# Performance work log

Hardware: AMD Instinct MI355X
Metric: run time of the kernel (lower is better)

The kernel has to match this reference:

```python
import jax, jax.numpy as jnp
import numpy as np

N_NODES = 100000


def spmm(edge_src, edge_dst, edge_val, x):
    """z[dst] += val * x[src] over all edges (COO sparse-dense matmul)."""
    gathered = edge_val[:, None] * x[edge_src]  # [E, d]
    return jax.ops.segment_sum(gathered, edge_dst, num_segments=N_NODES)


def setup_inputs() -> dict:
    key = jax.random.key(0)
    k1, k2, k3, k4, k5, k6 = jax.random.split(key, 6)
    N, E, IN, H, C = N_NODES, 1600000, 256, 128, 40
    features = jax.random.normal(k1, (N, IN), dtype=jnp.float32)
    # xavier_uniform-like init
    b1 = float(np.sqrt(6.0 / (IN + H)))
    b2 = float(np.sqrt(6.0 / (H + C)))
    W1 = jax.random.uniform(k2, (IN, H), dtype=jnp.float32, minval=-b1, maxval=b1)
    W2 = jax.random.uniform(k3, (H, C), dtype=jnp.float32, minval=-b2, maxval=b2)
    edge_src = jax.random.randint(k4, (E,), 0, N, dtype=jnp.int32)
    edge_dst = jnp.sort(jax.random.randint(k5, (E,), 0, N, dtype=jnp.int32))
    # normalized-adjacency-like positive edge weights
    edge_val = jax.random.uniform(k6, (E,), dtype=jnp.float32)
    return {"features": features, "W1": W1, "W2": W2,
            "edge_src": edge_src, "edge_dst": edge_dst, "edge_val": edge_val}


def reference(features, W1, W2, edge_src, edge_dst, edge_val):
    # Decoupled GCN: all dense NN layers first (relu between, none after last) ...
    h = jax.nn.relu(features @ W1)
    h = h @ W2  # [N, num_classes]
    # ... then nlayers (=2) rounds of graph propagation (spmm aggregation)
    h = spmm(edge_src, edge_dst, edge_val, h)
    h = spmm(edge_src, edge_dst, edge_val, h)
    return h
```

## Files before the change

kernel.cpp:

```cpp
#include <hip/hip_runtime.h>
#include <cstddef>
#include <cstdint>

#define IN_DIM 256
#define H_DIM  128
#define C_DIM  40
#define BM     128
#define LDQ    68
#define XA_C   32
#define XB_C   8
#define STEP   512

typedef short bf16x8 __attribute__((ext_vector_type(8)));
typedef float f32x16 __attribute__((ext_vector_type(16)));
typedef uint  u32x4  __attribute__((ext_vector_type(4)));

__device__ __forceinline__ ushort f2bf(float f) {
  uint u = __builtin_bit_cast(uint, f);
  u += 0x7fffu + ((u >> 16) & 1u);
  return (ushort)(u >> 16);
}
__device__ __forceinline__ float bf2f(uint s) {
  uint u = s << 16;
  return __builtin_bit_cast(float, u);
}
__device__ __forceinline__ uint pack2bf(float a, float b) {
#if __has_builtin(__builtin_amdgcn_cvt_pk_bf16_f32)
  typedef __bf16 bf16v2 __attribute__((ext_vector_type(2)));
  bf16v2 r = __builtin_amdgcn_cvt_pk_bf16_f32(a, b);
  return __builtin_bit_cast(uint, r);
#else
  return (uint)f2bf(a) | ((uint)f2bf(b) << 16);
#endif
}

__global__ void setup_kernel(const int* __restrict__ dst, int E,
                             int* __restrict__ row_ptr, int N,
                             const float* __restrict__ W1,
                             const float* __restrict__ W2,
                             ushort* __restrict__ b_frag,
                             ushort* __restrict__ w2f) {
  int tid = blockIdx.x * blockDim.x + threadIdx.x;
  if (tid < E) {
    int d1 = dst[tid];
    int d0 = (tid == 0) ? -1 : dst[tid - 1];
    for (int v = d0 + 1; v <= d1; ++v) row_ptr[v] = tid;
    if (tid == E - 1)
      for (int v = d1 + 1; v <= N; ++v) row_ptr[v] = E;
    return;
  }
  int u = tid - E;
  if (u < 4096) {
    int l = u & 63, ks = (u >> 6) & 15, tn = u >> 10;
    int n  = 32 * tn + (l & 31);
    int k0 = ks * 16 + ((l >> 5) << 3);
    ushort r[8];
#pragma unroll
    for (int j = 0; j < 8; ++j) r[j] = f2bf(W1[(k0 + j) * H_DIM + n]);
    *(uint4*)(b_frag + u * 8) = *(uint4*)r;
    return;
  }
  u -= 4096;
  if (u < 1024) {
    int l = u & 63, kt = u >> 6;
    int tn = kt & 1, kb = kt >> 1;
    int n  = 32 * tn + (l & 31);
    int k0 = kb * 16 + ((l >> 5) << 3);
    ushort r[8];
#pragma unroll
    for (int j = 0; j < 8; ++j)
      r[j] = (n < C_DIM) ? f2bf(W2[(k0 + j) * C_DIM + n]) : (ushort)0;
    *(uint4*)(w2f + u * 8) = *(uint4*)r;
  }
}

__global__ __launch_bounds__(256, 4) void fused_dense_kernel(
    const float* __restrict__ feat, const ushort* __restrict__ b_frag,
    const ushort* __restrict__ w2f, ushort* __restrict__ z0a,
    ushort* __restrict__ z0b, int N) {
  __shared__ __align__(16) ushort smem[4 * 32 * LDQ];

  const int t = threadIdx.x;
  const int w = t >> 6, l = t & 63;
  const int nb = blockIdx.x * BM;
  ushort* slab = smem + w * (32 * LDQ);

  const int sr = l >> 4;
  const int sc = l & 15;

  f32x16 acc[4];
#pragma unroll
  for (int tn = 0; tn < 4; ++tn)
#pragma unroll
    for (int r = 0; r < 16; ++r) acc[tn][r] = 0.f;

  const ushort* bp = b_frag + l * 8;
  bf16x8 Bx[2][4];
#pragma unroll
  for (int tn = 0; tn < 4; ++tn)
    Bx[0][tn] = *(const bf16x8*)(bp + tn * (16 * STEP));

  const float* fbase = feat + (size_t)(nb + 32 * w) * IN_DIM + sc * 4;

  float4 pre[8];
#pragma unroll
  for (int c = 0; c < 8; ++c) {
    int grow = nb + 32 * w + 4 * c + sr;
    const float* p = fbase + (size_t)(4 * c + sr) * IN_DIM;
    if (grow >= N) p = feat + (size_t)(N - 1) * IN_DIM + sc * 4;
    pre[c] = *(const float4*)(p);
  }
#pragma unroll
  for (int c = 0; c < 8; ++c) {
    uint2 pk;
    pk.x = pack2bf(pre[c].x, pre[c].y);
    pk.y = pack2bf(pre[c].z, pre[c].w);
    *(uint2*)(slab + (4 * c + sr) * LDQ + sc * 4) = pk;
  }

  const ushort* Abase = slab + (l & 31) * LDQ + ((l >> 5) << 3);

#pragma unroll
  for (int q = 0; q < 4; ++q) {
#pragma unroll
    for (int ks = 0; ks < 4; ++ks) {
      const int gks = 4 * q + ks;
      const int c = gks & 1;
      if (gks < 15) {
#pragma unroll
        for (int tn = 0; tn < 4; ++tn)
          Bx[c ^ 1][tn] = *(const bf16x8*)(bp + tn * (16 * STEP) + (gks + 1) * STEP);
      }
      if (q < 3) {
#pragma unroll
        for (int d = 0; d < 2; ++d) {
          const int cc = 2 * ks + d;
          int grow = nb + 32 * w + 4 * cc + sr;
          const float* p = fbase + (size_t)(4 * cc + sr) * IN_DIM + (q + 1) * 64;
          if (grow >= N) p = feat + (size_t)(N - 1) * IN_DIM + sc * 4 + (q + 1) * 64;
          pre[cc] = *(const float4*)(p);
        }
      }
      bf16x8 af = *(const bf16x8*)(Abase + ks * 16);
#pragma unroll
      for (int tn = 0; tn < 4; ++tn)
        acc[tn] = __builtin_amdgcn_mfma_f32_32x32x16_bf16(af, Bx[c][tn], acc[tn], 0, 0, 0);
    }
    if (q < 3) {
#pragma unroll
      for (int c = 0; c < 8; ++c) {
        uint2 pk;
        pk.x = pack2bf(pre[c].x, pre[c].y);
        pk.y = pack2bf(pre[c].z, pre[c].w);
        *(uint2*)(slab + (4 * c + sr) * LDQ + sc * 4) = pk;
      }
    }
  }

  f32x16 acc2[2];
#pragma unroll
  for (int tn = 0; tn < 2; ++tn)
#pragma unroll
    for (int r = 0; r < 16; ++r) acc2[tn][r] = 0.f;

  const ushort* Hbase = slab + (l & 31) * LDQ + ((l >> 5) << 3);
  const ushort* wp = w2f + l * 8;

#pragma unroll
  for (int hc = 0; hc < 2; ++hc) {
#pragma unroll
    for (int tn = 2 * hc; tn < 2 * hc + 2; ++tn) {
      int col = (tn - 2 * hc) * 32 + (l & 31);
#pragma unroll
      for (int r = 0; r < 16; ++r) {
        int nl = (r & 3) + 8 * (r >> 2) + 4 * (l >> 5);
        float v = acc[tn][r];
        slab[nl * LDQ + col] = f2bf(v > 0.f ? v : 0.f);
      }
    }
#pragma unroll
    for (int kb = 4 * hc; kb < 4 * hc + 4; ++kb) {
      bf16x8 af = *(const bf16x8*)(Hbase + (kb - 4 * hc) * 16);
#pragma unroll
      for (int tn = 0; tn < 2; ++tn) {
        bf16x8 bfr = *(const bf16x8*)(wp + (kb * 2 + tn) * STEP);
        acc2[tn] = __builtin_amdgcn_mfma_f32_32x32x16_bf16(af, bfr, acc2[tn], 0, 0, 0);
      }
    }
  }

#pragma unroll
  for (int r = 0; r < 16; ++r) {
    int node = nb + 32 * w + (r & 3) + 8 * (r >> 2) + 4 * (l >> 5);
    if (node < N) {
      z0a[(size_t)node * XA_C + (l & 31)] = f2bf(acc2[0][r]);
      if ((l & 31) < XB_C)
        z0b[(size_t)node * XB_C + (l & 31)] = f2bf(acc2[1][r]);
    }
  }
}

__global__ __launch_bounds__(256) void spmm_kernel(
    const int* __restrict__ row_ptr, const int* __restrict__ esrc,
    const float* __restrict__ eval, const ushort* __restrict__ xa,
    const ushort* __restrict__ xb, ushort* __restrict__ za,
    ushort* __restrict__ zb8, float* __restrict__ zf, int N, int out_f32) {
  int node = blockIdx.x * 8 + (threadIdx.x >> 5);
  if (node >= N) return;
  const int lh = threadIdx.x & 31;
  const int h = lh >> 2;
  const int j = lh & 3;

  int e   = row_ptr[node];
  int end = row_ptr[node + 1];

  float acc[8], accb[8];
#pragma unroll
  for (int c = 0; c < 8; ++c) { acc[c] = 0.f; accb[c] = 0.f; }

  for (; e + 16 <= end; e += 16) {
    int   s0 = esrc[e + h];
    int   s1 = esrc[e + 8 + h];
    float v0 = eval[e + h];
    float v1 = eval[e + 8 + h];
    u32x4 a = *(const u32x4*)(xa + (size_t)s0 * XA_C + j * 8);
    u32x4 b = *(const u32x4*)(xa + (size_t)s1 * XA_C + j * 8);
    acc[0] = fmaf(v0, bf2f(a.x & 0xffffu), acc[0]);
    acc[1] = fmaf(v0, bf2f(a.x >> 16),     acc[1]);
    acc[2] = fmaf(v0, bf2f(a.y & 0xffffu), acc[2]);
    acc[3] = fmaf(v0, bf2f(a.y >> 16),     acc[3]);
    acc[4] = fmaf(v0, bf2f(a.z & 0xffffu), acc[4]);
    acc[5] = fmaf(v0, bf2f(a.z >> 16),     acc[5]);
    acc[6] = fmaf(v0, bf2f(a.w & 0xffffu), acc[6]);
    acc[7] = fmaf(v0, bf2f(a.w >> 16),     acc[7]);
    acc[0] = fmaf(v1, bf2f(b.x & 0xffffu), acc[0]);
    acc[1] = fmaf(v1, bf2f(b.x >> 16),     acc[1]);
    acc[2] = fmaf(v1, bf2f(b.y & 0xffffu), acc[2]);
    acc[3] = fmaf(v1, bf2f(b.y >> 16),     acc[3]);
    acc[4] = fmaf(v1, bf2f(b.z & 0xffffu), acc[4]);
    acc[5] = fmaf(v1, bf2f(b.z >> 16),     acc[5]);
    acc[6] = fmaf(v1, bf2f(b.w & 0xffffu), acc[6]);
    acc[7] = fmaf(v1, bf2f(b.w >> 16),     acc[7]);
    if (j == 0) {
      u32x4 p = *(const u32x4*)(xb + (size_t)s0 * XB_C);
      u32x4 q = *(const u32x4*)(xb + (size_t)s1 * XB_C);
      accb[0] = fmaf(v0, bf2f(p.x & 0xffffu), accb[0]);
      accb[1] = fmaf(v0, bf2f(p.x >> 16),     accb[1]);
      accb[2] = fmaf(v0, bf2f(p.y & 0xffffu), accb[2]);
      accb[3] = fmaf(v0, bf2f(p.y >> 16),     accb[3]);
      accb[4] = fmaf(v0, bf2f(p.z & 0xffffu), accb[4]);
      accb[5] = fmaf(v0, bf2f(p.z >> 16),     accb[5]);
      accb[6] = fmaf(v0, bf2f(p.w & 0xffffu), accb[6]);
      accb[7] = fmaf(v0, bf2f(p.w >> 16),     accb[7]);
      accb[0] = fmaf(v1, bf2f(q.x & 0xffffu), accb[0]);
      accb[1] = fmaf(v1, bf2f(q.x >> 16),     accb[1]);
      accb[2] = fmaf(v1, bf2f(q.y & 0xffffu), accb[2]);
      accb[3] = fmaf(v1, bf2f(q.y >> 16),     accb[3]);
      accb[4] = fmaf(v1, bf2f(q.z & 0xffffu), accb[4]);
      accb[5] = fmaf(v1, bf2f(q.z >> 16),     accb[5]);
      accb[6] = fmaf(v1, bf2f(q.w & 0xffffu), accb[6]);
      accb[7] = fmaf(v1, bf2f(q.w >> 16),     accb[7]);
    }
  }
  for (; e + 8 <= end; e += 8) {
    int   s = esrc[e + h];
    float v = eval[e + h];
    u32x4 a = *(const u32x4*)(xa + (size_t)s * XA_C + j * 8);
    acc[0] = fmaf(v, bf2f(a.x & 0xffffu), acc[0]);
    acc[1] = fmaf(v, bf2f(a.x >> 16),     acc[1]);
    acc[2] = fmaf(v, bf2f(a.y & 0xffffu), acc[2]);
    acc[3] = fmaf(v, bf2f(a.y >> 16),     acc[3]);
    acc[4] = fmaf(v, bf2f(a.z & 0xffffu), acc[4]);
    acc[5] = fmaf(v, bf2f(a.z >> 16),     acc[5]);
    acc[6] = fmaf(v, bf2f(a.w & 0xffffu), acc[6]);
    acc[7] = fmaf(v, bf2f(a.w >> 16),     acc[7]);
    if (j == 0) {
      u32x4 p = *(const u32x4*)(xb + (size_t)s * XB_C);
      accb[0] = fmaf(v, bf2f(p.x & 0xffffu), accb[0]);
      accb[1] = fmaf(v, bf2f(p.x >> 16),     accb[1]);
      accb[2] = fmaf(v, bf2f(p.y & 0xffffu), accb[2]);
      accb[3] = fmaf(v, bf2f(p.y >> 16),     accb[3]);
      accb[4] = fmaf(v, bf2f(p.z & 0xffffu), accb[4]);
      accb[5] = fmaf(v, bf2f(p.z >> 16),     accb[5]);
      accb[6] = fmaf(v, bf2f(p.w & 0xffffu), accb[6]);
      accb[7] = fmaf(v, bf2f(p.w >> 16),     accb[7]);
    }
  }
  if (e < end) {
    int ei = e + h;
    int ec = ei < end ? ei : end - 1;
    int   s  = esrc[ec];
    float v0 = eval[ec];
    float v  = ei < end ? v0 : 0.f;
    u32x4 a = *(const u32x4*)(xa + (size_t)s * XA_C + j * 8);
    acc[0] = fmaf(v, bf2f(a.x & 0xffffu), acc[0]);
    acc[1] = fmaf(v, bf2f(a.x >> 16),     acc[1]);
    acc[2] = fmaf(v, bf2f(a.y & 0xffffu), acc[2]);
    acc[3] = fmaf(v, bf2f(a.y >> 16),     acc[3]);
    acc[4] = fmaf(v, bf2f(a.z & 0xffffu), acc[4]);
    acc[5] = fmaf(v, bf2f(a.z >> 16),     acc[5]);
    acc[6] = fmaf(v, bf2f(a.w & 0xffffu), acc[6]);
    acc[7] = fmaf(v, bf2f(a.w >> 16),     acc[7]);
    if (j == 0) {
      u32x4 p = *(const u32x4*)(xb + (size_t)s * XB_C);
      accb[0] = fmaf(v, bf2f(p.x & 0xffffu), accb[0]);
      accb[1] = fmaf(v, bf2f(p.x >> 16),     accb[1]);
      accb[2] = fmaf(v, bf2f(p.y & 0xffffu), accb[2]);
      accb[3] = fmaf(v, bf2f(p.y >> 16),     accb[3]);
      accb[4] = fmaf(v, bf2f(p.z & 0xffffu), accb[4]);
      accb[5] = fmaf(v, bf2f(p.z >> 16),     accb[5]);
      accb[6] = fmaf(v, bf2f(p.w & 0xffffu), accb[6]);
      accb[7] = fmaf(v, bf2f(p.w >> 16),     accb[7]);
    }
  }

#pragma unroll
  for (int c = 0; c < 8; ++c) { acc[c] += __shfl_xor(acc[c], 4);  accb[c] += __shfl_xor(accb[c], 4); }
#pragma unroll
  for (int c = 0; c < 8; ++c) { acc[c] += __shfl_xor(acc[c], 8);  accb[c] += __shfl_xor(accb[c], 8); }
#pragma unroll
  for (int c = 0; c < 8; ++c) { acc[c] += __shfl_xor(acc[c], 16); accb[c] += __shfl_xor(accb[c], 16); }

  if (out_f32) {
    if (h == 0) {
      float4 o0 = {acc[0], acc[1], acc[2], acc[3]};
      float4 o1 = {acc[4], acc[5], acc[6], acc[7]};
      float* p = zf + (size_t)node * C_DIM + j * 8;
      *(float4*)(p + 0) = o0;
      *(float4*)(p + 4) = o1;
      if (j == 0) {
        float4 b0 = {accb[0], accb[1], accb[2], accb[3]};
        float4 b1 = {accb[4], accb[5], accb[6], accb[7]};
        float* pb = zf + (size_t)node * C_DIM + 32;
        *(float4*)(pb + 0) = b0;
        *(float4*)(pb + 4) = b1;
      }
    }
  } else {
    if (h == 0) {
      uint4 p;
      p.x = (uint)f2bf(acc[0]) | ((uint)f2bf(acc[1]) << 16);
      p.y = (uint)f2bf(acc[2]) | ((uint)f2bf(acc[3]) << 16);
      p.z = (uint)f2bf(acc[4]) | ((uint)f2bf(acc[5]) << 16);
      p.w = (uint)f2bf(acc[6]) | ((uint)f2bf(acc[7]) << 16);
      *(uint4*)(za + (size_t)node * XA_C + j * 8) = p;
      if (j == 0) {
        uint4 q;
        q.x = (uint)f2bf(accb[0]) | ((uint)f2bf(accb[1]) << 16);
        q.y = (uint)f2bf(accb[2]) | ((uint)f2bf(accb[3]) << 16);
        q.z = (uint)f2bf(accb[4]) | ((uint)f2bf(accb[5]) << 16);
        q.w = (uint)f2bf(accb[6]) | ((uint)f2bf(accb[7]) << 16);
        *(uint4*)(zb8 + (size_t)node * XB_C) = q;
      }
    }
  }
}

extern "C" void kernel_launch(void* const* d_in, const int* in_sizes, int n_in,
                              void* d_out, int out_size, void* d_ws, size_t ws_size,
                              hipStream_t stream) {
  const float* feat  = (const float*)d_in[0];
  const float* W1    = (const float*)d_in[1];
  const float* W2    = (const float*)d_in[2];
  const int*   esrc  = (const int*)d_in[3];
  const int*   edst  = (const int*)d_in[4];
  const float* evalp = (const float*)d_in[5];
  float* out = (float*)d_out;

  const int N = in_sizes[0] / IN_DIM;
  const int E = in_sizes[3];

  const int nblk = (N + BM - 1) / BM;

  char* ws = (char*)d_ws;
  ushort* z0a    = (ushort*)ws;
  ushort* z0b    = z0a + (size_t)N * XA_C;
  ushort* z1a    = z0b + (size_t)N * XB_C;
  ushort* z1b    = z1a + (size_t)N * XA_C;
  ushort* b_frag = z1b + (size_t)N * XB_C;
  ushort* w2f    = b_frag + 4 * 16 * STEP;
  int* row_ptr   = (int*)(w2f + 16 * STEP);

  const int setup_items = E + 4096 + 1024;
  setup_kernel<<<(setup_items + 255) / 256, 256, 0, stream>>>(
      edst, E, row_ptr, N, W1, W2, b_frag, w2f);
  fused_dense_kernel<<<nblk, 256, 0, stream>>>(feat, b_frag, w2f, z0a, z0b, N);
  spmm_kernel<<<(N + 7) / 8, 256, 0, stream>>>(row_ptr, esrc, evalp, z0a, z0b,
                                               z1a, z1b, nullptr, N, 0);
  spmm_kernel<<<(N + 7) / 8, 256, 0, stream>>>(row_ptr, esrc, evalp, z1a, z1b,
                                               nullptr, nullptr, out, N, 1);
}
```

Measured before the change: 267.9 us.

## Stage W1/W2 bf16 fragments in LDS instead of per-wave global loads

The dense kernel now copies the pre-swizzled W1 fragments (in two halves of 16 k-steps worth) and the W2 fragments into shared memory once per block, and each wave reads B operands from LDS instead of global/L2. The W1 fragment layout is reordered so that each half is contiguous, and the feature prefetch is restructured to load a whole 64-column chunk ahead. This cuts redundant global traffic for the weights across the four waves, but adds block-wide barriers, LDS use of about 66 KB, and a drop in launch bounds occupancy from 4 to 2 blocks per CU.

New measurement: 267.9 us. No clear change (-0.0%).

```diff
diff --git a/kernel.cpp b/kernel.cpp
--- a/kernel.cpp
+++ b/kernel.cpp
@@ -10,6 +10,8 @@
 #define XA_C   32
 #define XB_C   8
 #define STEP   512
+#define B_OFF  (4 * 32 * LDQ)
+#define W2_OFF (B_OFF + 16384)
 
 typedef short bf16x8 __attribute__((ext_vector_type(8)));
 typedef float f32x16 __attribute__((ext_vector_type(16)));
@@ -51,7 +53,7 @@
   }
   int u = tid - E;
   if (u < 4096) {
-    int l = u & 63, ks = (u >> 6) & 15, tn = u >> 10;
+    int l = u & 63, tn = (u >> 6) & 3, ks = u >> 8;
     int n  = 32 * tn + (l & 31);
     int k0 = ks * 16 + ((l >> 5) << 3);
     ushort r[8];
@@ -74,11 +76,11 @@
   }
 }
 
-__global__ __launch_bounds__(256, 4) void fused_dense_kernel(
+__global__ __launch_bounds__(256, 2) void fused_dense_kernel(
     const float* __restrict__ feat, const ushort* __restrict__ b_frag,
     const ushort* __restrict__ w2f, ushort* __restrict__ z0a,
     ushort* __restrict__ z0b, int N) {
-  __shared__ __align__(16) ushort smem[4 * 32 * LDQ];
+  __shared__ __align__(16) ushort smem[33280];
 
   const int t = threadIdx.x;
   const int w = t >> 6, l = t & 63;
@@ -94,14 +96,16 @@
 #pragma unroll
     for (int r = 0; r < 16; ++r) acc[tn][r] = 0.f;
 
-  const ushort* bp = b_frag + l * 8;
-  bf16x8 Bx[2][4];
-#pragma unroll
-  for (int tn = 0; tn < 4; ++tn)
-    Bx[0][tn] = *(const bf16x8*)(bp + tn * (16 * STEP));
+#pragma unroll
+  for (int i = 0; i < 8; ++i)
+    *(uint4*)(smem + B_OFF + t * 64 + i * 8) =
+        *(const uint4*)(b_frag + t * 64 + i * 8);
+#pragma unroll
+  for (int i = 0; i < 4; ++i)
+    *(uint4*)(smem + W2_OFF + t * 32 + i * 8) =
+        *(const uint4*)(w2f + t * 32 + i * 8);
 
   const float* fbase = feat + (size_t)(nb + 32 * w) * IN_DIM + sc * 4;
-
   float4 pre[8];
 #pragma unroll
   for (int c = 0; c < 8; ++c) {
@@ -117,34 +121,36 @@
     pk.y = pack2bf(pre[c].z, pre[c].w);
     *(uint2*)(slab + (4 * c + sr) * LDQ + sc * 4) = pk;
   }
+#pragma unroll
+  for (int c = 0; c < 8; ++c) {
+    int grow = nb + 32 * w + 4 * c + sr;
+    const float* p = fbase + (size_t)(4 * c + sr) * IN_DIM + 64;
+    if (grow >= N) p = feat + (size_t)(N - 1) * IN_DIM + sc * 4 + 64;
+    pre[c] = *(const float4*)(p);
+  }
+  __syncthreads();
 
   const ushort* Abase = slab + (l & 31) * LDQ + ((l >> 5) << 3);
 
 #pragma unroll
   for (int q = 0; q < 4; ++q) {
-#pragma unroll
-    for (int ks = 0; ks < 4; ++ks) {
-      const int gks = 4 * q + ks;
-      const int c = gks & 1;
-      if (gks < 15) {
-#pragma unroll
-        for (int tn = 0; tn < 4; ++tn)
-          Bx[c ^ 1][tn] = *(const bf16x8*)(bp + tn * (16 * STEP) + (gks + 1) * STEP);
-      }
-      if (q < 3) {
-#pragma unroll
-        for (int d = 0; d < 2; ++d) {
-          const int cc = 2 * ks + d;
-          int grow = nb + 32 * w + 4 * cc + sr;
-          const float* p = fbase + (size_t)(4 * cc + sr) * IN_DIM + (q + 1) * 64;
-          if (grow >= N) p = feat + (size_t)(N - 1) * IN_DIM + sc * 4 + (q + 1) * 64;
-          pre[cc] = *(const float4*)(p);
-        }
-      }
-      bf16x8 af = *(const bf16x8*)(Abase + ks * 16);
-#pragma unroll
-      for (int tn = 0; tn < 4; ++tn)
-        acc[tn] = __builtin_amdgcn_mfma_f32_32x32x16_bf16(af, Bx[c][tn], acc[tn], 0, 0, 0);
+    if (q == 2) {
+      __syncthreads();
+#pragma unroll
+      for (int i = 0; i < 8; ++i)
+        *(uint4*)(smem + B_OFF + t * 64 + i * 8) =
+            *(const uint4*)(b_frag + 16384 + t * 64 + i * 8);
+      __syncthreads();
+    }
+#pragma unroll
+    for (int ksl = 0; ksl < 4; ++ksl) {
+      const int gks = 4 * q + ksl;
+      bf16x8 af = *(const bf16x8*)(Abase + ksl * 16);
+#pragma unroll
+      for (int tn = 0; tn < 4; ++tn) {
+        bf16x8 bfr = *(const bf16x8*)(smem + B_OFF + ((gks & 7) * 256 + tn * 64 + l) * 8);
+        acc[tn] = __builtin_amdgcn_mfma_f32_32x32x16_bf16(af, bfr, acc[tn], 0, 0, 0);
+      }
     }
     if (q < 3) {
 #pragma unroll
@@ -154,6 +160,15 @@
         pk.y = pack2bf(pre[c].z, pre[c].w);
         *(uint2*)(slab + (4 * c + sr) * LDQ + sc * 4) = pk;
       }
+      if (q < 2) {
+#pragma unroll
+        for (int c = 0; c < 8; ++c) {
+          int grow = nb + 32 * w + 4 * c + sr;
+          const float* p = fbase + (size_t)(4 * c + sr) * IN_DIM + (q + 2) * 64;
+          if (grow >= N) p = feat + (size_t)(N - 1) * IN_DIM + sc * 4 + (q + 2) * 64;
+          pre[c] = *(const float4*)(p);
+        }
+      }
     }
   }
 
@@ -162,9 +177,6 @@
   for (int tn = 0; tn < 2; ++tn)
 #pragma unroll
     for (int r = 0; r < 16; ++r) acc2[tn][r] = 0.f;
-
-  const ushort* Hbase = slab + (l & 31) * LDQ + ((l >> 5) << 3);
-  const ushort* wp = w2f + l * 8;
 
 #pragma unroll
   for (int hc = 0; hc < 2; ++hc) {
@@ -180,10 +192,10 @@
     }
 #pragma unroll
     for (int kb = 4 * hc; kb < 4 * hc + 4; ++kb) {
-      bf16x8 af = *(const bf16x8*)(Hbase + (kb - 4 * hc) * 16);
+      bf16x8 af = *(const bf16x8*)(Abase + (kb - 4 * hc) * 16);
 #pragma unroll
       for (int tn = 0; tn < 2; ++tn) {
-        bf16x8 bfr = *(const bf16x8*)(wp + (kb * 2 + tn) * STEP);
+        bf16x8 bfr = *(const bf16x8*)(smem + W2_OFF + (kb * 2 + tn) * 512 + l * 8);
         acc2[tn] = __builtin_amdgcn_mfma_f32_32x32x16_bf16(af, bfr, acc2[tn], 0, 0, 0);
       }
     }
```
